# Performance work log

Measured on AMD Instinct MI355X. Metric: run time of the kernel, lower is better.

## Reference

```python
import jax, jax.numpy as jnp
import numpy as np

N_SLOTS = 524288
DIM_MEM = 128
DIM_IN = 1024
SHIFT_RADIUS = 3
EPS = 1e-8  # torch cosine_similarity eps


def setup_inputs() -> dict:
    key = jax.random.key(0)
    k1, k2, k3, k4, k5 = jax.random.split(key, 5)
    n_factors = DIM_MEM + 1 + 1 + (2 * SHIFT_RADIUS + 1) + 1  # 138
    return {
        "input_from_controller": jax.random.normal(k1, (DIM_IN,), dtype=jnp.float32),
        "previous_weighting": jax.random.uniform(k2, (N_SLOTS,), dtype=jnp.float32),
        "memory": jax.random.normal(k3, (N_SLOTS, DIM_MEM), dtype=jnp.float32),
        "W_wf": jax.random.normal(k4, (DIM_IN, n_factors), dtype=jnp.float32) * 0.02,
        "b_wf": jax.random.normal(k5, (n_factors,), dtype=jnp.float32) * 0.02,
    }


def _get_weighting(input_from_controller, previous_weighting, memory, W_wf, b_wf):
    factors = input_from_controller @ W_wf + b_wf  # [138]
    M = DIM_MEM
    key_v = factors[:M]                       # [M]
    key_s = factors[M]                        # scalar (beta)
    gate = jax.nn.softmax(factors[M + 1:M + 2])      # size-1 softmax -> 1.0 (faithful)
    shift_w = jax.nn.softmax(factors[M + 2:M + 2 + 2 * SHIFT_RADIUS + 1])  # [2r+1]
    sharpening = jax.nn.relu(factors[-1]) + 1.0

    # content addressing: cosine similarity of each memory row with key_v
    mem_norm = jnp.maximum(jnp.linalg.norm(memory, axis=1), EPS)  # [N]
    key_norm = jnp.maximum(jnp.linalg.norm(key_v), EPS)
    content_w = (memory @ key_v) / (mem_norm * key_norm)          # [N]
    content_w = jax.nn.softmax(key_s * content_w)

    gated_w = content_w * gate[0] + (1.0 - gate[0]) * previous_weighting

    # circular convolution: shifted[i] = sum_j gated[(i - r + j) % N] * shift_w[j]
    shifted_w = jnp.zeros_like(gated_w)
    for j in range(2 * SHIFT_RADIUS + 1):  # small fixed tap count (7)
        shifted_w = shifted_w + shift_w[j] * jnp.roll(gated_w, SHIFT_RADIUS - j)

    pw = shifted_w ** sharpening
    return pw / pw.sum()


def reference(input_from_controller, previous_weighting, memory, W_wf, b_wf):
    w = _get_weighting(input_from_controller, previous_weighting, memory, W_wf, b_wf)
    read_vector = w @ memory  # read head forward
    return read_vector
```

## Files before the change

kernel.cpp:

```cpp
#include <hip/hip_runtime.h>
#include <math.h>

#define N_SLOTS 524288
#define DIM_MEM 128
#define DIM_IN 1024
#define NFACT 138
#define EPSF 1e-8f

#define SB 2048
#define SIT 32

#define CPB 4
#define ROWS_PC 64
#define NPAIR 70
#define PAD 33

#define WS_NEED ((size_t)4096 + (size_t)N_SLOTS * 4 + (size_t)(DIM_MEM + 1) * SB * 4)

__global__ __launch_bounds__(256) void k_factors(const float* __restrict__ x,
                                                 const float* __restrict__ W,
                                                 const float* __restrict__ b,
                                                 float* __restrict__ factors) {
    int j = threadIdx.x;
    int i0 = blockIdx.x * 32;
    if (j < NFACT) {
        float acc = 0.f;
        #pragma unroll 8
        for (int i = i0; i < i0 + 32; ++i)
            acc = fmaf(x[i], W[(size_t)i * NFACT + j], acc);
        if (blockIdx.x == 0) acc += b[j];
        atomicAdd(&factors[j], acc);
    }
}

__global__ void k_derived(const float* __restrict__ f, float* __restrict__ d) {
    int l = threadIdx.x;
    float v = f[l] * f[l] + f[l + 64] * f[l + 64];
    for (int off = 32; off; off >>= 1) v += __shfl_xor(v, off, 64);
    if (l == 0) {
        float key_norm = fmaxf(sqrtf(v), EPSF);
        d[0] = f[128] / key_norm;
        float m = f[130];
        for (int j = 1; j < 7; ++j) m = fmaxf(m, f[130 + j]);
        float e[7], s = 0.f;
        for (int j = 0; j < 7; ++j) { e[j] = expf(f[130 + j] - m); s += e[j]; }
        for (int j = 0; j < 7; ++j) d[1 + j] = e[j] / s;
        d[8] = fmaxf(f[137], 0.f) + 1.f;
    }
}

__global__ __launch_bounds__(256) void k_score(const float* __restrict__ mem,
                                               const float* __restrict__ keyv,
                                               const float* __restrict__ der,
                                               float* __restrict__ e_out) {
    const int tid  = threadIdx.x;
    const int lane = tid & 31;
    const int hw   = tid >> 5;
    const float4* __restrict__ mem4 = (const float4*)mem;
    const float4 k4 = ((const float4*)keyv)[lane];
    const float d0 = der[0];

    int r = blockIdx.x * (SIT * 8) + hw;
    const float4* __restrict__ p = mem4 + (size_t)r * 32 + lane;

    #pragma unroll 4
    for (int it = 0; it < SIT; ++it, r += 8, p += 8 * 32) {
        float4 m = *p;
        float dp = m.x * k4.x + m.y * k4.y + m.z * k4.z + m.w * k4.w;
        float np = m.x * m.x + m.y * m.y + m.z * m.z + m.w * m.w;
        #pragma unroll
        for (int off = 16; off; off >>= 1) {
            dp += __shfl_xor(dp, off, 32);
            np += __shfl_xor(np, off, 32);
        }
        if (lane == 0)
            e_out[r] = __expf(d0 * dp / fmaxf(sqrtf(np), EPSF));
    }
}

__global__ __launch_bounds__(256) void k_readout(const float* __restrict__ mem,
                                                 const float* __restrict__ e,
                                                 const float* __restrict__ der,
                                                 float* __restrict__ sc) {
    __shared__ float colpart[8][DIM_MEM];
    __shared__ float psum[8];

    const int tid  = threadIdx.x;
    const int lane = tid & 31;
    const int hw   = tid >> 5;
    const float4* __restrict__ mem4 = (const float4*)mem;
    const float sharp = der[8];
    float sw[7];
    #pragma unroll
    for (int d = 0; d < 7; ++d) sw[d] = der[1 + d];

    float4 acc = make_float4(0.f, 0.f, 0.f, 0.f);
    float wsum = 0.f;

    int r = blockIdx.x * (SIT * 8) + hw;
    const float4* __restrict__ p = mem4 + (size_t)r * 32 + lane;

    #pragma unroll 2
    for (int it = 0; it < SIT; ++it, r += 8, p += 8 * 32) {
        float4 m = *p;
        float t = 0.f;
        #pragma unroll
        for (int d = 0; d < 7; ++d)
            t = fmaf(sw[d], e[(r + d - 3) & (N_SLOTS - 1)], t);
        float w = __expf(sharp * __logf(t));
        acc.x = fmaf(w, m.x, acc.x);
        acc.y = fmaf(w, m.y, acc.y);
        acc.z = fmaf(w, m.z, acc.z);
        acc.w = fmaf(w, m.w, acc.w);
        if (lane == 0) wsum += w;
    }

    ((float4*)colpart[hw])[lane] = acc;
    if (lane == 0) psum[hw] = wsum;
    __syncthreads();
    if (tid < DIM_MEM) {
        float s = 0.f;
        #pragma unroll
        for (int h = 0; h < 8; ++h) s += colpart[h][tid];
        sc[(size_t)tid * SB + blockIdx.x] = s;
    }
    if (tid == 0) {
        float s = 0.f;
        #pragma unroll
        for (int h = 0; h < 8; ++h) s += psum[h];
        sc[(size_t)DIM_MEM * SB + blockIdx.x] = s;
    }
}

__global__ void k_reduce(const float* __restrict__ sc, float* __restrict__ out) {
    __shared__ float red[8];
    const int c = blockIdx.x;
    const int t = threadIdx.x;
    float s = 0.f, pv = 0.f;
    for (int b = t; b < SB; b += 256) {
        s  += sc[(size_t)c * SB + b];
        pv += sc[(size_t)DIM_MEM * SB + b];
    }
    #pragma unroll
    for (int off = 32; off; off >>= 1) {
        s  += __shfl_xor(s, off, 64);
        pv += __shfl_xor(pv, off, 64);
    }
    const int w = t >> 6;
    if ((t & 63) == 0) { red[w * 2] = s; red[w * 2 + 1] = pv; }
    __syncthreads();
    if (t == 0) {
        float S = 0.f, P = 0.f;
        #pragma unroll
        for (int i = 0; i < 4; ++i) { S += red[i * 2]; P += red[i * 2 + 1]; }
        out[c] = S / P;
    }
}

__global__ __launch_bounds__(256) void k_main(const float* __restrict__ mem,
                                              const float* __restrict__ keyv,
                                              const float* __restrict__ der,
                                              float* __restrict__ num,
                                              double* __restrict__ P_acc) {
    __shared__ float part[2 * NPAIR * PAD];
    __shared__ float sums[2 * NPAIR];
    __shared__ float e_sh[NPAIR];
    __shared__ float w_sh[ROWS_PC];
    __shared__ float colpart[8][DIM_MEM];
    __shared__ float psum[8];

    const int tid  = threadIdx.x;
    const int lane = tid & 31;
    const int hw   = tid >> 5;
    const float4* mem4 = (const float4*)mem;
    const float4 k4 = ((const float4*)keyv)[lane];
    const float d0 = der[0];
    const float sharp = der[8];
    float sw[7];
    #pragma unroll
    for (int d = 0; d < 7; ++d) sw[d] = der[1 + d];

    float4 acc = make_float4(0.f, 0.f, 0.f, 0.f);
    float wsum = 0.f;

    for (int c = 0; c < CPB; ++c) {
        const int r0 = blockIdx.x * (CPB * ROWS_PC) + c * ROWS_PC;
        const int rbase = r0 + hw * 8;
        float4 row[8];
        #pragma unroll
        for (int j = 0; j < 8; ++j)
            row[j] = mem4[(size_t)(rbase + j) * 32 + lane];
        #pragma unroll
        for (int j = 0; j < 8; ++j) {
            float dp = row[j].x * k4.x + row[j].y * k4.y + row[j].z * k4.z + row[j].w * k4.w;
            float np = row[j].x * row[j].x + row[j].y * row[j].y + row[j].z * row[j].z + row[j].w * row[j].w;
            int pp = 3 + hw * 8 + j;
            part[(pp * 2 + 0) * PAD + lane] = dp;
            part[(pp * 2 + 1) * PAD + lane] = np;
        }
        if (hw < 6) {
            int hr = (hw < 3) ? (r0 - 3 + hw) : (r0 + ROWS_PC + (hw - 3));
            hr &= (N_SLOTS - 1);
            int pp = (hw < 3) ? hw : (64 + hw);
            float4 m4 = mem4[(size_t)hr * 32 + lane];
            part[(pp * 2 + 0) * PAD + lane] =
                m4.x * k4.x + m4.y * k4.y + m4.z * k4.z + m4.w * k4.w;
            part[(pp * 2 + 1) * PAD + lane] =
                m4.x * m4.x + m4.y * m4.y + m4.z * m4.z + m4.w * m4.w;
        }
        __syncthreads();
        if (tid < 2 * NPAIR) {
            float s = 0.f;
            #pragma unroll
            for (int l = 0; l < 32; ++l) s += part[tid * PAD + l];
            sums[tid] = s;
        }
        __syncthreads();
        if (tid < NPAIR) {
            float dot = sums[tid * 2], n2 = sums[tid * 2 + 1];
            e_sh[tid] = __expf(d0 * dot / fmaxf(sqrtf(n2), EPSF));
        }
        __syncthreads();
        if (tid < ROWS_PC) {
            float t = 0.f;
            #pragma unroll
            for (int d = 0; d < 7; ++d) t = fmaf(sw[d], e_sh[tid + d], t);
            w_sh[tid] = __expf(sharp * __logf(t));
        }
        __syncthreads();
        #pragma unroll
        for (int j = 0; j < 8; ++j) {
            float w = w_sh[hw * 8 + j];
            acc.x = fmaf(w, row[j].x, acc.x);
            acc.y = fmaf(w, row[j].y, acc.y);
            acc.z = fmaf(w, row[j].z, acc.z);
            acc.w = fmaf(w, row[j].w, acc.w);
            wsum += w;
        }
        __syncthreads();
    }

    ((float4*)colpart[hw])[lane] = acc;
    if (lane == 0) psum[hw] = wsum;
    __syncthreads();
    if (tid < DIM_MEM) {
        float s = 0.f;
        #pragma unroll
        for (int h = 0; h < 8; ++h) s += colpart[h][tid];
        atomicAdd(&num[tid], s);
    }
    if (tid == 0) {
        float s = 0.f;
        #pragma unroll
        for (int h = 0; h < 8; ++h) s += psum[h];
        atomicAdd(P_acc, (double)s);
    }
}

__global__ void k_final(const float* __restrict__ num,
                        const double* __restrict__ P_acc,
                        float* __restrict__ out) {
    out[threadIdx.x] = num[threadIdx.x] / (float)(*P_acc);
}

extern "C" void kernel_launch(void* const* d_in, const int* in_sizes, int n_in,
                              void* d_out, int out_size, void* d_ws, size_t ws_size,
                              hipStream_t stream) {
    const float* x   = (const float*)d_in[0];
    const float* mem = (const float*)d_in[2];
    const float* W   = (const float*)d_in[3];
    const float* b   = (const float*)d_in[4];
    float* out = (float*)d_out;

    char* ws = (char*)d_ws;
    float* factors = (float*)ws;
    float* derived = (float*)(ws + 1024);

    hipMemsetAsync(ws, 0, 4096, stream);

    k_factors<<<DIM_IN / 32, 256, 0, stream>>>(x, W, b, factors);
    k_derived<<<1, 64, 0, stream>>>(factors, derived);

    if (ws_size >= WS_NEED) {
        float* e  = (float*)(ws + 4096);
        float* sc = (float*)(ws + 4096 + (size_t)N_SLOTS * 4);
        k_score<<<SB, 256, 0, stream>>>(mem, factors, derived, e);
        k_readout<<<SB, 256, 0, stream>>>(mem, e, derived, sc);
        k_reduce<<<DIM_MEM, 256, 0, stream>>>(sc, out);
    } else {
        double* P_acc = (double*)(ws + 2048);
        float*  num   = (float*)(ws + 2176);
        k_main<<<N_SLOTS / (CPB * ROWS_PC), 256, 0, stream>>>(mem, factors, derived, num, P_acc);
        k_final<<<1, DIM_MEM, 0, stream>>>(num, P_acc, out);
    }
}
```

Baseline: 418.9 us.

## Fuse scoring and readout into one pass over memory with halo rows

Replaces the separate score and readout kernels, which each streamed the full memory matrix, with one kernel that computes cosine scores, the shift convolution and the weighted accumulation per 64-row chunk in shared memory. Halo rows are recomputed to cover neighbouring taps, and the next chunk is register-prefetched. The derived-parameter computation is folded into the fused kernel, and the factor GEMV becomes a per-output block reduction without a memset or atomics. This trades extra halo loads and per-chunk barriers for roughly halving global memory traffic and dropping several launches.

```diff
diff --git a/kernel.cpp b/kernel.cpp
--- a/kernel.cpp
+++ b/kernel.cpp
@@ -7,112 +7,142 @@
 #define NFACT 138
 #define EPSF 1e-8f
 
-#define SB 2048
-#define SIT 32
-
-#define CPB 4
-#define ROWS_PC 64
-#define NPAIR 70
-#define PAD 33
-
-#define WS_NEED ((size_t)4096 + (size_t)N_SLOTS * 4 + (size_t)(DIM_MEM + 1) * SB * 4)
+#define RPB 256
+#define CHUNK 64
+#define NCH (RPB / CHUNK)
+#define FB (N_SLOTS / RPB)
+
+#define WS_NEED ((size_t)4096 + (size_t)(DIM_MEM + 1) * FB * 4)
 
 __global__ __launch_bounds__(256) void k_factors(const float* __restrict__ x,
                                                  const float* __restrict__ W,
                                                  const float* __restrict__ b,
                                                  float* __restrict__ factors) {
-    int j = threadIdx.x;
-    int i0 = blockIdx.x * 32;
-    if (j < NFACT) {
-        float acc = 0.f;
-        #pragma unroll 8
-        for (int i = i0; i < i0 + 32; ++i)
-            acc = fmaf(x[i], W[(size_t)i * NFACT + j], acc);
-        if (blockIdx.x == 0) acc += b[j];
-        atomicAdd(&factors[j], acc);
-    }
-}
-
-__global__ void k_derived(const float* __restrict__ f, float* __restrict__ d) {
-    int l = threadIdx.x;
-    float v = f[l] * f[l] + f[l + 64] * f[l + 64];
-    for (int off = 32; off; off >>= 1) v += __shfl_xor(v, off, 64);
-    if (l == 0) {
-        float key_norm = fmaxf(sqrtf(v), EPSF);
-        d[0] = f[128] / key_norm;
-        float m = f[130];
-        for (int j = 1; j < 7; ++j) m = fmaxf(m, f[130 + j]);
-        float e[7], s = 0.f;
-        for (int j = 0; j < 7; ++j) { e[j] = expf(f[130 + j] - m); s += e[j]; }
-        for (int j = 0; j < 7; ++j) d[1 + j] = e[j] / s;
-        d[8] = fmaxf(f[137], 0.f) + 1.f;
-    }
-}
-
-__global__ __launch_bounds__(256) void k_score(const float* __restrict__ mem,
-                                               const float* __restrict__ keyv,
-                                               const float* __restrict__ der,
-                                               float* __restrict__ e_out) {
+    __shared__ float wred[4];
+    const int j = blockIdx.x;
+    const int t = threadIdx.x;
+    float acc = 0.f;
+    #pragma unroll
+    for (int i = t; i < DIM_IN; i += 256)
+        acc = fmaf(x[i], W[(size_t)i * NFACT + j], acc);
+    #pragma unroll
+    for (int off = 32; off; off >>= 1) acc += __shfl_xor(acc, off, 64);
+    if ((t & 63) == 0) wred[t >> 6] = acc;
+    __syncthreads();
+    if (t == 0)
+        factors[j] = wred[0] + wred[1] + wred[2] + wred[3] + b[j];
+}
+
+__global__ __launch_bounds__(256) void k_fused(const float* __restrict__ mem,
+                                               const float* __restrict__ f,
+                                               float* __restrict__ sc) {
+    __shared__ float d_sh[12];
+    __shared__ float e_sh[CHUNK + 8];
+    __shared__ float w_sh[CHUNK];
+    __shared__ float colpart[8][DIM_MEM];
+    __shared__ float psum[8];
+
     const int tid  = threadIdx.x;
     const int lane = tid & 31;
     const int hw   = tid >> 5;
+
+    if (tid < 64) {
+        float fl = f[tid], fh = f[tid + 64];
+        float v = fl * fl + fh * fh;
+        #pragma unroll
+        for (int off = 32; off; off >>= 1) v += __shfl_xor(v, off, 64);
+        if (tid == 0) {
+            float key_norm = fmaxf(sqrtf(v), EPSF);
+            d_sh[0] = f[128] / key_norm;
+            float m = f[130];
+            #pragma unroll
+            for (int q = 1; q < 7; ++q) m = fmaxf(m, f[130 + q]);
+            float e[7], s = 0.f;
+            #pragma unroll
+            for (int q = 0; q < 7; ++q) { e[q] = __expf(f[130 + q] - m); s += e[q]; }
+            #pragma unroll
+            for (int q = 0; q < 7; ++q) d_sh[1 + q] = e[q] / s;
+            d_sh[8] = fmaxf(f[137], 0.f) + 1.f;
+        }
+    }
+    __syncthreads();
+
     const float4* __restrict__ mem4 = (const float4*)mem;
-    const float4 k4 = ((const float4*)keyv)[lane];
-    const float d0 = der[0];
-
-    int r = blockIdx.x * (SIT * 8) + hw;
-    const float4* __restrict__ p = mem4 + (size_t)r * 32 + lane;
-
-    #pragma unroll 4
-    for (int it = 0; it < SIT; ++it, r += 8, p += 8 * 32) {
-        float4 m = *p;
-        float dp = m.x * k4.x + m.y * k4.y + m.z * k4.z + m.w * k4.w;
-        float np = m.x * m.x + m.y * m.y + m.z * m.z + m.w * m.w;
-        #pragma unroll
-        for (int off = 16; off; off >>= 1) {
-            dp += __shfl_xor(dp, off, 32);
-            np += __shfl_xor(np, off, 32);
-        }
-        if (lane == 0)
-            e_out[r] = __expf(d0 * dp / fmaxf(sqrtf(np), EPSF));
-    }
-}
-
-__global__ __launch_bounds__(256) void k_readout(const float* __restrict__ mem,
-                                                 const float* __restrict__ e,
-                                                 const float* __restrict__ der,
-                                                 float* __restrict__ sc) {
-    __shared__ float colpart[8][DIM_MEM];
-    __shared__ float psum[8];
-
-    const int tid  = threadIdx.x;
-    const int lane = tid & 31;
-    const int hw   = tid >> 5;
-    const float4* __restrict__ mem4 = (const float4*)mem;
-    const float sharp = der[8];
+    const float4 k4 = ((const float4*)f)[lane];
+    const float d0 = d_sh[0];
+    const float sharp = d_sh[8];
     float sw[7];
     #pragma unroll
-    for (int d = 0; d < 7; ++d) sw[d] = der[1 + d];
+    for (int d = 0; d < 7; ++d) sw[d] = d_sh[1 + d];
 
     float4 acc = make_float4(0.f, 0.f, 0.f, 0.f);
     float wsum = 0.f;
-
-    int r = blockIdx.x * (SIT * 8) + hw;
-    const float4* __restrict__ p = mem4 + (size_t)r * 32 + lane;
-
-    #pragma unroll 2
-    for (int it = 0; it < SIT; ++it, r += 8, p += 8 * 32) {
-        float4 m = *p;
-        float t = 0.f;
-        #pragma unroll
-        for (int d = 0; d < 7; ++d)
-            t = fmaf(sw[d], e[(r + d - 3) & (N_SLOTS - 1)], t);
-        float w = __expf(sharp * __logf(t));
-        acc.x = fmaf(w, m.x, acc.x);
-        acc.y = fmaf(w, m.y, acc.y);
-        acc.z = fmaf(w, m.z, acc.z);
-        acc.w = fmaf(w, m.w, acc.w);
-        if (lane == 0) wsum += w;
+    const int base = blockIdx.x * RPB;
+
+    float4 row[2][8];
+    #pragma unroll
+    for (int j = 0; j < 8; ++j)
+        row[0][j] = mem4[(size_t)(base + hw * 8 + j) * 32 + lane];
+
+    #pragma unroll
+    for (int c = 0; c < NCH; ++c) {
+        const int cur = c & 1;
+        const int nxt = cur ^ 1;
+        const int r0 = base + c * CHUNK;
+
+        #pragma unroll
+        for (int j = 0; j < 8; ++j) {
+            float4 m = row[cur][j];
+            float dp = m.x * k4.x + m.y * k4.y + m.z * k4.z + m.w * k4.w;
+            float np = m.x * m.x + m.y * m.y + m.z * m.z + m.w * m.w;
+            #pragma unroll
+            for (int off = 16; off; off >>= 1) {
+                dp += __shfl_xor(dp, off, 32);
+                np += __shfl_xor(np, off, 32);
+            }
+            if (lane == 0)
+                e_sh[3 + hw * 8 + j] = __expf(d0 * dp / fmaxf(sqrtf(np), EPSF));
+        }
+        if (hw < 6) {
+            int hr = (hw < 3) ? (r0 - 3 + hw) : (r0 + CHUNK + (hw - 3));
+            hr &= (N_SLOTS - 1);
+            const int p = (hw < 3) ? hw : (CHUNK + hw);
+            float4 m = mem4[(size_t)hr * 32 + lane];
+            float dp = m.x * k4.x + m.y * k4.y + m.z * k4.z + m.w * k4.w;
+            float np = m.x * m.x + m.y * m.y + m.z * m.z + m.w * m.w;
+            #pragma unroll
+            for (int off = 16; off; off >>= 1) {
+                dp += __shfl_xor(dp, off, 32);
+                np += __shfl_xor(np, off, 32);
+            }
+            if (lane == 0)
+                e_sh[p] = __expf(d0 * dp / fmaxf(sqrtf(np), EPSF));
+        }
+        if (c + 1 < NCH) {
+            const int nb = r0 + CHUNK + hw * 8;
+            #pragma unroll
+            for (int j = 0; j < 8; ++j)
+                row[nxt][j] = mem4[(size_t)(nb + j) * 32 + lane];
+        }
+        __syncthreads();
+
+        if (tid < CHUNK) {
+            float t = 0.f;
+            #pragma unroll
+            for (int d = 0; d < 7; ++d) t = fmaf(sw[d], e_sh[tid + d], t);
+            w_sh[tid] = __expf(sharp * __logf(t));
+        }
+        __syncthreads();
+
+        #pragma unroll
+        for (int j = 0; j < 8; ++j) {
+            float w = w_sh[hw * 8 + j];
+            acc.x = fmaf(w, row[cur][j].x, acc.x);
+            acc.y = fmaf(w, row[cur][j].y, acc.y);
+            acc.z = fmaf(w, row[cur][j].z, acc.z);
+            acc.w = fmaf(w, row[cur][j].w, acc.w);
+            wsum += w;
+        }
     }
 
     ((float4*)colpart[hw])[lane] = acc;
@@ -122,13 +152,13 @@
         float s = 0.f;
         #pragma unroll
         for (int h = 0; h < 8; ++h) s += colpart[h][tid];
-        sc[(size_t)tid * SB + blockIdx.x] = s;
+        sc[(size_t)tid * FB + blockIdx.x] = s;
     }
     if (tid == 0) {
         float s = 0.f;
         #pragma unroll
         for (int h = 0; h < 8; ++h) s += psum[h];
-        sc[(size_t)DIM_MEM * SB + blockIdx.x] = s;
+        sc[(size_t)DIM_MEM * FB + blockIdx.x] = s;
     }
 }
 
@@ -137,9 +167,9 @@
     const int c = blockIdx.x;
     const int t = threadIdx.x;
     float s = 0.f, pv = 0.f;
-    for (int b = t; b < SB; b += 256) {
-        s  += sc[(size_t)c * SB + b];
-        pv += sc[(size_t)DIM_MEM * SB + b];
+    for (int b = t; b < FB; b += 256) {
+        s  += sc[(size_t)c * FB + b];
+        pv += sc[(size_t)DIM_MEM * FB + b];
     }
     #pragma unroll
     for (int off = 32; off; off >>= 1) {
@@ -157,140 +187,21 @@
     }
 }
 
-__global__ __launch_bounds__(256) void k_main(const float* __restrict__ mem,
-                                              const float* __restrict__ keyv,
-                                              const float* __restrict__ der,
-                                              float* __restrict__ num,
-                                              double* __restrict__ P_acc) {
-    __shared__ float part[2 * NPAIR * PAD];
-    __shared__ float sums[2 * NPAIR];
-    __shared__ float e_sh[NPAIR];
-    __shared__ float w_sh[ROWS_PC];
-    __shared__ float colpart[8][DIM_MEM];
-    __shared__ float psum[8];
-
-    const int tid  = threadIdx.x;
-    const int lane = tid & 31;
-    const int hw   = tid >> 5;
-    const float4* mem4 = (const float4*)mem;
-    const float4 k4 = ((const float4*)keyv)[lane];
-    const float d0 = der[0];
-    const float sharp = der[8];
-    float sw[7];
-    #pragma unroll
-    for (int d = 0; d < 7; ++d) sw[d] = der[1 + d];
-
-    float4 acc = make_float4(0.f, 0.f, 0.f, 0.f);
-    float wsum = 0.f;
-
-    for (int c = 0; c < CPB; ++c) {
-        const int r0 = blockIdx.x * (CPB * ROWS_PC) + c * ROWS_PC;
-        const int rbase = r0 + hw * 8;
-        float4 row[8];
-        #pragma unroll
-        for (int j = 0; j < 8; ++j)
-            row[j] = mem4[(size_t)(rbase + j) * 32 + lane];
-        #pragma unroll
-        for (int j = 0; j < 8; ++j) {
-            float dp = row[j].x * k4.x + row[j].y * k4.y + row[j].z * k4.z + row[j].w * k4.w;
-            float np = row[j].x * row[j].x + row[j].y * row[j].y + row[j].z * row[j].z + row[j].w * row[j].w;
-            int pp = 3 + hw * 8 + j;
-            part[(pp * 2 + 0) * PAD + lane] = dp;
-            part[(pp * 2 + 1) * PAD + lane] = np;
-        }
-        if (hw < 6) {
-            int hr = (hw < 3) ? (r0 - 3 + hw) : (r0 + ROWS_PC + (hw - 3));
-            hr &= (N_SLOTS - 1);
-            int pp = (hw < 3) ? hw : (64 + hw);
-            float4 m4 = mem4[(size_t)hr * 32 + lane];
-            part[(pp * 2 + 0) * PAD + lane] =
-                m4.x * k4.x + m4.y * k4.y + m4.z * k4.z + m4.w * k4.w;
-            part[(pp * 2 + 1) * PAD + lane] =
-                m4.x * m4.x + m4.y * m4.y + m4.z * m4.z + m4.w * m4.w;
-        }
-        __syncthreads();
-        if (tid < 2 * NPAIR) {
-            float s = 0.f;
-            #pragma unroll
-            for (int l = 0; l < 32; ++l) s += part[tid * PAD + l];
-            sums[tid] = s;
-        }
-        __syncthreads();
-        if (tid < NPAIR) {
-            float dot = sums[tid * 2], n2 = sums[tid * 2 + 1];
-            e_sh[tid] = __expf(d0 * dot / fmaxf(sqrtf(n2), EPSF));
-        }
-        __syncthreads();
-        if (tid < ROWS_PC) {
-            float t = 0.f;
-            #pragma unroll
-            for (int d = 0; d < 7; ++d) t = fmaf(sw[d], e_sh[tid + d], t);
-            w_sh[tid] = __expf(sharp * __logf(t));
-        }
-        __syncthreads();
-        #pragma unroll
-        for (int j = 0; j < 8; ++j) {
-            float w = w_sh[hw * 8 + j];
-            acc.x = fmaf(w, row[j].x, acc.x);
-            acc.y = fmaf(w, row[j].y, acc.y);
-            acc.z = fmaf(w, row[j].z, acc.z);
-            acc.w = fmaf(w, row[j].w, acc.w);
-            wsum += w;
-        }
-        __syncthreads();
-    }
-
-    ((float4*)colpart[hw])[lane] = acc;
-    if (lane == 0) psum[hw] = wsum;
-    __syncthreads();
-    if (tid < DIM_MEM) {
-        float s = 0.f;
-        #pragma unroll
-        for (int h = 0; h < 8; ++h) s += colpart[h][tid];
-        atomicAdd(&num[tid], s);
-    }
-    if (tid == 0) {
-        float s = 0.f;
-        #pragma unroll
-        for (int h = 0; h < 8; ++h) s += psum[h];
-        atomicAdd(P_acc, (double)s);
-    }
-}
-
-__global__ void k_final(const float* __restrict__ num,
-                        const double* __restrict__ P_acc,
-                        float* __restrict__ out) {
-    out[threadIdx.x] = num[threadIdx.x] / (float)(*P_acc);
-}
-
 extern "C" void kernel_launch(void* const* d_in, const int* in_sizes, int n_in,
                               void* d_out, int out_size, void* d_ws, size_t ws_size,
                               hipStream_t stream) {
+    (void)in_sizes; (void)n_in; (void)out_size; (void)ws_size;
     const float* x   = (const float*)d_in[0];
     const float* mem = (const float*)d_in[2];
     const float* W   = (const float*)d_in[3];
     const float* b   = (const float*)d_in[4];
     float* out = (float*)d_out;
 
-    char* ws = (char*)d_ws;
+    char*  ws      = (char*)d_ws;
     float* factors = (float*)ws;
-    float* derived = (float*)(ws + 1024);
-
-    hipMemsetAsync(ws, 0, 4096, stream);
-
-    k_factors<<<DIM_IN / 32, 256, 0, stream>>>(x, W, b, factors);
-    k_derived<<<1, 64, 0, stream>>>(factors, derived);
-
-    if (ws_size >= WS_NEED) {
-        float* e  = (float*)(ws + 4096);
-        float* sc = (float*)(ws + 4096 + (size_t)N_SLOTS * 4);
-        k_score<<<SB, 256, 0, stream>>>(mem, factors, derived, e);
-        k_readout<<<SB, 256, 0, stream>>>(mem, e, derived, sc);
-        k_reduce<<<DIM_MEM, 256, 0, stream>>>(sc, out);
-    } else {
-        double* P_acc = (double*)(ws + 2048);
-        float*  num   = (float*)(ws + 2176);
-        k_main<<<N_SLOTS / (CPB * ROWS_PC), 256, 0, stream>>>(mem, factors, derived, num, P_acc);
-        k_final<<<1, DIM_MEM, 0, stream>>>(num, P_acc, out);
-    }
-}
+    float* sc      = (float*)(ws + 4096);
+
+    k_factors<<<NFACT, 256, 0, stream>>>(x, W, b, factors);
+    k_fused<<<FB, 256, 0, stream>>>(mem, factors, sc);
+    k_reduce<<<DIM_MEM, 256, 0, stream>>>(sc, out);
+}
```

After: 381.5 us. 1.1x faster.
